# Performance work log

Measured on AMD Instinct MI355X. Metric: run time of the kernel, lower is better.

## Reference

```python
import jax, jax.numpy as jnp
import numpy as np

B, Q, P, H, NH, NKV, D = 8, 16, 4096, 4096, 32, 8, 128
ROPE_BASE = 10000.0


def setup_inputs() -> dict:
    key = jax.random.key(0)
    ks = jax.random.split(key, 8)
    hidden_states = jax.random.normal(ks[0], (B, Q, H), dtype=jnp.float32)
    past_key = jax.random.normal(ks[1], (B, NKV, P, D), dtype=jnp.float32)
    past_value = jax.random.normal(ks[2], (B, NKV, P, D), dtype=jnp.float32)
    # draft tokens continue right after the cached prefix
    position_ids = jnp.broadcast_to(P + jnp.arange(Q, dtype=jnp.int64), (B, Q))
    attention_bias = jnp.zeros((B, 1, Q, P + Q), dtype=jnp.float32)
    s = 0.02
    Wq = jax.random.normal(ks[3], (H, NH * D), dtype=jnp.float32) * s
    Wk = jax.random.normal(ks[4], (H, NKV * D), dtype=jnp.float32) * s
    Wv = jax.random.normal(ks[5], (H, NKV * D), dtype=jnp.float32) * s
    Wo = jax.random.normal(ks[6], (NH * D, H), dtype=jnp.float32) * s
    return {"hidden_states": hidden_states, "position_ids": position_ids,
            "past_key": past_key, "past_value": past_value,
            "attention_bias": attention_bias, "Wq": Wq, "Wk": Wk, "Wv": Wv, "Wo": Wo}


def _rope_cos_sin(position_ids, dtype):
    # inv_freq over even dims, GPT-NeoX layout: angles repeated (concat) over halves
    inv_freq = 1.0 / (ROPE_BASE ** (jnp.arange(0, D, 2, dtype=jnp.float32) / D))
    ang = position_ids.astype(jnp.float32)[:, :, None] * inv_freq  # [B,Q,D/2]
    emb = jnp.concatenate([ang, ang], axis=-1)  # [B,Q,D]
    cos = jnp.cos(emb).astype(dtype)[:, None, :, :]  # [B,1,Q,D]
    sin = jnp.sin(emb).astype(dtype)[:, None, :, :]
    return cos, sin


def _rotate_half(x):
    x1, x2 = jnp.split(x, 2, axis=-1)
    return jnp.concatenate([-x2, x1], axis=-1)


def reference(hidden_states, position_ids, past_key, past_value, attention_bias,
              Wq, Wk, Wv, Wo):
    b, q_len, _ = hidden_states.shape
    n_kv = past_key.shape[1]
    groups = NH // n_kv
    # projections
    q = (hidden_states @ Wq).reshape(b, q_len, NH, D).transpose(0, 2, 1, 3)   # [B,NH,Q,D]
    k = (hidden_states @ Wk).reshape(b, q_len, n_kv, D).transpose(0, 2, 1, 3)  # [B,NKV,Q,D]
    v = (hidden_states @ Wv).reshape(b, q_len, n_kv, D).transpose(0, 2, 1, 3)
    # RoPE
    cos, sin = _rope_cos_sin(position_ids, hidden_states.dtype)
    q = q * cos + _rotate_half(q) * sin
    k = k * cos + _rotate_half(k) * sin
    # KV-cache append
    k_all = jnp.concatenate([past_key, k], axis=2)    # [B,NKV,S,D]
    v_all = jnp.concatenate([past_value, v], axis=2)
    # GQA attention: group query heads per kv head instead of repeat_interleave
    qg = q.reshape(b, n_kv, groups, q_len, D)
    scale = 1.0 / jnp.sqrt(jnp.asarray(D, dtype=hidden_states.dtype))
    scores = jnp.einsum('bkgqd,bksd->bkgqs', qg, k_all) * scale
    scores = scores + attention_bias[:, :, None, :, :]  # bias [B,1,Q,S] -> broadcast
    probs = jax.nn.softmax(scores, axis=-1)
    out = jnp.einsum('bkgqs,bksd->bkgqd', probs, v_all)  # [B,NKV,G,Q,D]
    out = out.reshape(b, NH, q_len, D).transpose(0, 2, 1, 3).reshape(b, q_len, NH * D)
    return out @ Wo
```

## Files before the change

### kernel.cpp

```cpp
#include <hip/hip_runtime.h>
#include <hip/hip_bf16.h>

#define NB 8
#define NQ 16
#define NP 4096
#define NHID 4096
#define NHEADS 32
#define NKVH 8
#define NG 4
#define ND 128
#define NM 128
#define NSEQ 4112
#define N_QKV 6144
#define SPLITK 8
#define NS 8

typedef __attribute__((ext_vector_type(8))) short bf16x8;
typedef __attribute__((ext_vector_type(4))) float f32x4;

__device__ __forceinline__ unsigned short f2bf(float f) {
  unsigned int u = __float_as_uint(f);
  u = (u + 0x7FFFu + ((u >> 16) & 1u)) >> 16;
  return (unsigned short)u;
}

__device__ __forceinline__ unsigned cvtpk(float lo, float hi) {
  unsigned r;
  asm("v_cvt_pk_bf16_f32 %0, %1, %2" : "=v"(r) : "v"(lo), "v"(hi));
  return r;
}

__device__ __forceinline__ float bf2f(unsigned short u) {
  return __uint_as_float(((unsigned)u) << 16);
}

#define TRREAD(dst, a32) \
  asm volatile("ds_read_b64_tr_b16 %0, %1" : "=v"(dst) : "v"(a32))
#define LGKM0() asm volatile("s_waitcnt lgkmcnt(0)" ::: "memory")
#define SBAR()                              \
  do {                                      \
    __builtin_amdgcn_sched_barrier(0);      \
    __builtin_amdgcn_s_barrier();           \
    __builtin_amdgcn_sched_barrier(0);      \
  } while (0)

__global__ __launch_bounds__(256) void k_cvt(const float* __restrict__ x,
                                             unsigned short* __restrict__ y, int n4) {
  int i = blockIdx.x * 256 + threadIdx.x;
  if (i >= n4) return;
  f32x4 v = ((const f32x4*)x)[i];
  uint2 o;
  o.x = cvtpk(v[0], v[1]);
  o.y = cvtpk(v[2], v[3]);
  ((uint2*)y)[i] = o;
}

template<int CT>
__global__ __launch_bounds__(256) void k_gemm(
    const unsigned short* __restrict__ A, int lda,
    const float* __restrict__ W0, const float* __restrict__ W1,
    const float* __restrict__ W2, int nw0, int nw1, int N, int KS,
    float* __restrict__ part) {
  constexpr int BN = CT * 32;
  constexpr int NT = CT * 2;
  constexpr int NW4 = BN / 4;
  constexpr int KST = 256 / NW4;
  __shared__ __align__(16) char Bl[8 * NT * 128];
  int n0 = blockIdx.x * BN;
  int k0 = blockIdx.y * KS;
  const float* Wp; int ldw, ncol;
  if (n0 < nw0)      { Wp = W0; ldw = nw0;       ncol = n0; }
  else if (n0 < nw1) { Wp = W1; ldw = nw1 - nw0; ncol = n0 - nw0; }
  else               { Wp = W2; ldw = N - nw1;   ncol = n0 - nw1; }
  int tid = threadIdx.x, lane = tid & 63, wid = tid >> 6;
  int r16 = lane & 15, hi = lane >> 4;
  int wr = wid >> 1, wc = wid & 1;
  int n4 = tid & (NW4 - 1), krow = tid / NW4;
  unsigned lb = (unsigned)(uintptr_t)(void*)Bl;

  f32x4 acc[4][CT];
#pragma unroll
  for (int i = 0; i < 4; ++i)
#pragma unroll
    for (int j = 0; j < CT; ++j) acc[i][j] = {0.f, 0.f, 0.f, 0.f};

  f32x4 cur[CT], nxt[CT];
#pragma unroll
  for (int r = 0; r < CT; ++r) {
    cur[r] = *(const f32x4*)&Wp[(size_t)(k0 + krow + r * KST) * ldw + ncol + n4 * 4];
    nxt[r] = cur[r];
  }

  for (int kk = 0; kk < KS; kk += 32) {
    SBAR();
    if (kk + 32 < KS) {
#pragma unroll
      for (int r = 0; r < CT; ++r)
        nxt[r] = *(const f32x4*)&Wp[(size_t)(k0 + kk + 32 + krow + r * KST) * ldw + ncol + n4 * 4];
    }
#pragma unroll
    for (int r = 0; r < CT; ++r) {
      int k = krow + r * KST;
      uint2 u;
      u.x = cvtpk(cur[r][0], cur[r][1]);
      u.y = cvtpk(cur[r][2], cur[r][3]);
      *(uint2*)(Bl + ((k >> 2) * NT + (n4 >> 2)) * 128 + (k & 3) * 32 + (n4 & 3) * 8) = u;
    }
    LGKM0();
    SBAR();
    bf16x8 af[4];
#pragma unroll
    for (int rt = 0; rt < 4; ++rt)
      af[rt] = *(const bf16x8*)&A[(size_t)(wr * 64 + rt * 16 + r16) * lda + k0 + kk + hi * 8];
    unsigned long long rr[2 * CT];
#pragma unroll
    for (int ct = 0; ct < CT; ++ct) {
      int s1 = hi * (2 * NT) + wc * CT + ct;
      TRREAD(rr[ct * 2],     lb + s1 * 128 + r16 * 8);
      TRREAD(rr[ct * 2 + 1], lb + (s1 + NT) * 128 + r16 * 8);
    }
    LGKM0();
    __builtin_amdgcn_sched_barrier(0);
    __builtin_amdgcn_s_setprio(1);
#pragma unroll
    for (int ct = 0; ct < CT; ++ct) {
      union { unsigned long long u[2]; bf16x8 v; } cc;
      cc.u[0] = rr[ct * 2]; cc.u[1] = rr[ct * 2 + 1];
#pragma unroll
      for (int rt = 0; rt < 4; ++rt)
        acc[rt][ct] = __builtin_amdgcn_mfma_f32_16x16x32_bf16(af[rt], cc.v, acc[rt][ct], 0, 0, 0);
    }
    __builtin_amdgcn_s_setprio(0);
#pragma unroll
    for (int r = 0; r < CT; ++r) cur[r] = nxt[r];
  }
  float* po = part + (size_t)blockIdx.y * NM * N;
#pragma unroll
  for (int rt = 0; rt < 4; ++rt)
#pragma unroll
    for (int ct = 0; ct < CT; ++ct)
#pragma unroll
      for (int r = 0; r < 4; ++r) {
        int m = wr * 64 + rt * 16 + hi * 4 + r;
        int n = n0 + wc * CT * 16 + ct * 16 + r16;
        po[(size_t)m * N + n] = acc[rt][ct][r];
      }
}

__global__ __launch_bounds__(256) void k_rope(
    const float* __restrict__ part, const void* __restrict__ posv,
    unsigned short* __restrict__ qb, unsigned short* __restrict__ kb,
    unsigned short* __restrict__ vb) {
  int t = blockIdx.x * 256 + threadIdx.x;
  int d = t & 63;
  int rest = t >> 6;
  int h = rest % 48;
  int m = rest / 48;
  if (m >= NM) return;
  const int* p32 = (const int*)posv;
  const long long* p64 = (const long long*)posv;
  bool is64 = (p64[0] == (long long)p32[0]);
  int pos = is64 ? (int)p64[m] : p32[m];
  int b = m >> 4, q = m & 15;

  int c1, c2;
  if (h < 32)      { c1 = h * ND + d; }
  else if (h < 40) { c1 = NHID + (h - 32) * ND + d; }
  else             { c1 = NHID + 1024 + (h - 40) * ND + d; }
  c2 = c1 + 64;
  float x1 = 0.f, x2 = 0.f;
#pragma unroll
  for (int c = 0; c < SPLITK; ++c) {
    x1 += part[((size_t)c * NM + m) * N_QKV + c1];
    x2 += part[((size_t)c * NM + m) * N_QKV + c2];
  }
  if (h < 40) {
    float invf = __expf(-(float)d * 0.14391156831212787f);
    float th = (float)pos * invf;
    float cs = cosf(th), sn = sinf(th);
    float o1 = x1 * cs - x2 * sn;
    float o2 = x2 * cs + x1 * sn;
    if (h < 32) {
      o1 *= 0.08838834764831845f;
      o2 *= 0.08838834764831845f;
      int kv = h >> 2, g = h & 3;
      size_t base = ((((size_t)b * NKVH + kv) * NG + g) * NQ + q) * ND;
      qb[base + d] = f2bf(o1);
      qb[base + d + 64] = f2bf(o2);
    } else {
      int kvh = h - 32;
      size_t base = (((size_t)b * NKVH + kvh) * NQ + q) * ND;
      kb[base + d] = f2bf(o1);
      kb[base + d + 64] = f2bf(o2);
    }
  } else {
    int kvh = h - 40;
    size_t base = (((size_t)b * NKVH + kvh) * NQ + q) * ND;
    vb[base + d] = f2bf(x1);
    vb[base + d + 64] = f2bf(x2);
  }
}

template<int NSPL>
__global__ __launch_bounds__(256, 2) void k_attn(
    const unsigned short* __restrict__ qb, const unsigned short* __restrict__ kb,
    const unsigned short* __restrict__ vb, const float* __restrict__ pastK,
    const float* __restrict__ pastV, const float* __restrict__ bias,
    unsigned short* __restrict__ pout, float* __restrict__ pml) {
  __shared__ __align__(16) char lds[73728];
  char* Pl = lds + 65536;
  constexpr int KEYS = NP / NSPL;
  constexpr int NSUB = KEYS / 64;
  int bkv = blockIdx.x;
  int split = blockIdx.y;
  int b = bkv >> 3, kv = bkv & 7;
  int tid = threadIdx.x, lane = tid & 63, wid = tid >> 6;
  int r16 = lane & 15, hi = lane >> 4;

  const unsigned short* qbase = qb + ((((size_t)b * NKVH + kv) * NG + wid) * NQ) * ND;
  bf16x8 qf[4];
#pragma unroll
  for (int kd = 0; kd < 4; ++kd)
    qf[kd] = *(const bf16x8*)&qbase[r16 * ND + kd * 32 + hi * 8];

  float m_run[4], l_run[4];
  f32x4 oacc[8];
#pragma unroll
  for (int r = 0; r < 4; ++r) { m_run[r] = -1e30f; l_run[r] = 0.f; }
#pragma unroll
  for (int dt = 0; dt < 8; ++dt) oacc[dt] = {0.f, 0.f, 0.f, 0.f};

  int s0 = split * KEYS;
  const float* Kg = pastK + ((size_t)(b * NKVH + kv) * NP + s0) * ND;
  const float* Vg = pastV + ((size_t)(b * NKVH + kv) * NP + s0) * ND;
  const float* biasrow = bias + (size_t)(b * NQ) * NSEQ;
  int d4 = tid & 31, sr = tid >> 5;
  bool last = (split == NSPL - 1);

  f32x4 rwK[8], rwV[8];
  float bcur[16], bn[16], bt[4];
  bf16x8 tk, tv;

  f32x4 sc[4];
  auto qk_softmax = [&](char* Kl, const float* bv, bool tail) {
    __builtin_amdgcn_s_setprio(1);
#pragma unroll
    for (int ct = 0; ct < 4; ++ct) {
      f32x4 a = {0.f, 0.f, 0.f, 0.f};
      int s = ct * 16 + r16;
#pragma unroll
      for (int kd = 0; kd < 4; ++kd) {
        bf16x8 kf = *(const bf16x8*)(Kl + s * 256 + ((kd * 64 + hi * 16) ^ ((s & 7) << 4)));
        a = __builtin_amdgcn_mfma_f32_16x16x32_bf16(qf[kd], kf, a, 0, 0, 0);
      }
      sc[ct] = a;
    }
    __builtin_amdgcn_s_setprio(0);
#pragma unroll
    for (int ct = 0; ct < 4; ++ct)
#pragma unroll
      for (int r = 0; r < 4; ++r) {
        if (!tail)          sc[ct][r] += bv[ct * 4 + r];
        else if (ct == 0)   sc[ct][r] += bv[r];
        else                sc[ct][r] = -1e30f;
      }
    float mnew[4], fac[4], rs[4];
#pragma unroll
    for (int r = 0; r < 4; ++r) {
      float v = fmaxf(fmaxf(sc[0][r], sc[1][r]), fmaxf(sc[2][r], sc[3][r]));
      v = fmaxf(v, __shfl_xor(v, 1));
      v = fmaxf(v, __shfl_xor(v, 2));
      v = fmaxf(v, __shfl_xor(v, 4));
      v = fmaxf(v, __shfl_xor(v, 8));
      mnew[r] = fmaxf(m_run[r], v);
      fac[r] = __expf(m_run[r] - mnew[r]);
      m_run[r] = mnew[r];
      rs[r] = 0.f;
    }
#pragma unroll
    for (int ct = 0; ct < 4; ++ct)
#pragma unroll
      for (int r = 0; r < 4; ++r) {
        float p = __expf(sc[ct][r] - mnew[r]);
        rs[r] += p;
        int q = hi * 4 + r, j = ct * 16 + r16;
        *(unsigned short*)(Pl + wid * 2048 + q * 128 + ((j * 2) ^ ((q & 7) << 4))) = f2bf(p);
      }
#pragma unroll
    for (int r = 0; r < 4; ++r) {
      float s = rs[r];
      s += __shfl_xor(s, 1);
      s += __shfl_xor(s, 2);
      s += __shfl_xor(s, 4);
      s += __shfl_xor(s, 8);
      l_run[r] = l_run[r] * fac[r] + s;
    }
#pragma unroll
    for (int dt = 0; dt < 8; ++dt)
#pragma unroll
      for (int r = 0; r < 4; ++r) oacc[dt][r] *= fac[r];
  };

  auto pv = [&](char* Vl) {
    unsigned vb32 = (unsigned)(uintptr_t)(void*)Vl;
#pragma unroll
    for (int kt = 0; kt < 2; ++kt) {
      bf16x8 pa = *(const bf16x8*)(Pl + wid * 2048 + r16 * 128 +
                                   ((kt * 64 + hi * 16) ^ ((r16 & 7) << 4)));
#pragma unroll
      for (int dh = 0; dh < 2; ++dh) {
        unsigned long long rr[8];
#pragma unroll
        for (int dq = 0; dq < 4; ++dq) {
          int sA = hi * 16 + kt * 64 + dh * 4 + dq;
          TRREAD(rr[dq * 2],     vb32 + sA * 128 + r16 * 8);
          TRREAD(rr[dq * 2 + 1], vb32 + (sA + 8) * 128 + r16 * 8);
        }
        LGKM0();
        __builtin_amdgcn_sched_barrier(0);
        __builtin_amdgcn_s_setprio(1);
#pragma unroll
        for (int dq = 0; dq < 4; ++dq) {
          union { unsigned long long u[2]; bf16x8 v; } cc;
          cc.u[0] = rr[dq * 2]; cc.u[1] = rr[dq * 2 + 1];
          oacc[dh * 4 + dq] = __builtin_amdgcn_mfma_f32_16x16x32_bf16(pa, cc.v, oacc[dh * 4 + dq], 0, 0, 0);
        }
        __builtin_amdgcn_s_setprio(0);
      }
    }
  };

#pragma unroll
  for (int it = 0; it < 8; ++it)
    rwK[it] = *(const f32x4*)&Kg[(size_t)(sr + it * 8) * ND + d4 * 4];
#pragma unroll
  for (int it = 0; it < 8; ++it)
    rwV[it] = *(const f32x4*)&Vg[(size_t)(sr + it * 8) * ND + d4 * 4];
#pragma unroll
  for (int ct = 0; ct < 4; ++ct)
#pragma unroll
    for (int r = 0; r < 4; ++r)
      bcur[ct * 4 + r] = biasrow[(size_t)(hi * 4 + r) * NSEQ + s0 + ct * 16 + r16];
#pragma unroll
  for (int it = 0; it < 8; ++it) {
    int s = sr + it * 8;
    uint2 u;
    u.x = cvtpk(rwK[it][0], rwK[it][1]); u.y = cvtpk(rwK[it][2], rwK[it][3]);
    *(uint2*)(lds + s * 256 + ((d4 * 8) ^ ((s & 7) << 4))) = u;
  }
#pragma unroll
  for (int it = 0; it < 8; ++it) {
    int s = sr + it * 8;
    uint2 u;
    u.x = cvtpk(rwV[it][0], rwV[it][1]); u.y = cvtpk(rwV[it][2], rwV[it][3]);
    *(uint2*)(lds + 32768 + ((s >> 2) * 8 + (d4 >> 2)) * 128 + (s & 3) * 32 + (d4 & 3) * 8) = u;
  }
  LGKM0();

  int cur = 0;
  for (int sub = 0; sub < NSUB; ++sub) {
    bool pf = (sub + 1 < NSUB);
    if (pf) {
      const float* Kn = Kg + (size_t)(sub + 1) * 64 * ND;
      const float* Vn = Vg + (size_t)(sub + 1) * 64 * ND;
#pragma unroll
      for (int it = 0; it < 8; ++it)
        rwK[it] = *(const f32x4*)&Kn[(size_t)(sr + it * 8) * ND + d4 * 4];
#pragma unroll
      for (int it = 0; it < 8; ++it)
        rwV[it] = *(const f32x4*)&Vn[(size_t)(sr + it * 8) * ND + d4 * 4];
#pragma unroll
      for (int ct = 0; ct < 4; ++ct)
#pragma unroll
        for (int r = 0; r < 4; ++r)
          bn[ct * 4 + r] = biasrow[(size_t)(hi * 4 + r) * NSEQ + s0 + (sub + 1) * 64 + ct * 16 + r16];
    } else if (last) {
      int s = tid >> 4, d8 = tid & 15;
      const unsigned short* Kn = kb + (((size_t)b * NKVH + kv) * NQ) * ND;
      const unsigned short* Vn = vb + (((size_t)b * NKVH + kv) * NQ) * ND;
      tk = *(const bf16x8*)&Kn[s * ND + d8 * 8];
      tv = *(const bf16x8*)&Vn[s * ND + d8 * 8];
#pragma unroll
      for (int r = 0; r < 4; ++r)
        bt[r] = biasrow[(size_t)(hi * 4 + r) * NSEQ + NP + r16];
    }
    SBAR();
    qk_softmax(lds + cur * 16384, bcur, false);
    pv(lds + 32768 + cur * 16384);
    if (pf) {
#pragma unroll
      for (int it = 0; it < 8; ++it) {
        int s = sr + it * 8;
        uint2 u;
        u.x = cvtpk(rwK[it][0], rwK[it][1]); u.y = cvtpk(rwK[it][2], rwK[it][3]);
        *(uint2*)(lds + (cur ^ 1) * 16384 + s * 256 + ((d4 * 8) ^ ((s & 7) << 4))) = u;
      }
#pragma unroll
      for (int it = 0; it < 8; ++it) {
        int s = sr + it * 8;
        uint2 u;
        u.x = cvtpk(rwV[it][0], rwV[it][1]); u.y = cvtpk(rwV[it][2], rwV[it][3]);
        *(uint2*)(lds + 32768 + (cur ^ 1) * 16384 +
                  ((s >> 2) * 8 + (d4 >> 2)) * 128 + (s & 3) * 32 + (d4 & 3) * 8) = u;
      }
#pragma unroll
      for (int i = 0; i < 16; ++i) bcur[i] = bn[i];
      LGKM0();
      cur ^= 1;
    } else if (last) {
      int s = tid >> 4, d8 = tid & 15;
      *(bf16x8*)(lds + (cur ^ 1) * 16384 + s * 256 + ((d8 * 16) ^ ((s & 7) << 4))) = tk;
      *(bf16x8*)(lds + 32768 + (cur ^ 1) * 16384 +
                 ((s >> 2) * 8 + (d8 >> 1)) * 128 + (s & 3) * 32 + (d8 & 1) * 16) = tv;
      LGKM0();
      cur ^= 1;
    }
  }
  if (last) {
    SBAR();
    qk_softmax(lds + cur * 16384, bt, true);
    pv(lds + 32768 + cur * 16384);
  }

  SBAR();
  char* My = lds + wid * 4096;
#pragma unroll
  for (int dt = 0; dt < 8; ++dt)
#pragma unroll
    for (int r = 0; r < 4; ++r)
      *(unsigned short*)(My + (hi * 4 + r) * 256 + (dt * 16 + r16) * 2) = f2bf(oacc[dt][r]);
  LGKM0();
  size_t rowbase = ((size_t)(b * NKVH + kv) * NG + wid) * NQ;
  unsigned short* po = pout + ((size_t)split * (NB * NKVH * NG * NQ) + rowbase) * ND;
#pragma unroll
  for (int it = 0; it < 4; ++it) {
    int row = it * 4 + (lane >> 4);
    uint4 vv = *(uint4*)(My + row * 256 + r16 * 16);
    *(uint4*)&po[(size_t)row * ND + r16 * 8] = vv;
  }
  if (r16 == 0) {
#pragma unroll
    for (int r = 0; r < 4; ++r) {
      size_t idx = ((size_t)split * (NB * NKVH * NG * NQ) + rowbase + hi * 4 + r) * 2;
      pml[idx] = m_run[r];
      pml[idx + 1] = l_run[r];
    }
  }
}

template<int NSPL>
__global__ __launch_bounds__(256) void k_combine(
    const unsigned short* __restrict__ pout, const float* __restrict__ pml,
    unsigned short* __restrict__ Aatt) {
  const int NROW = NB * NKVH * NG * NQ;
  int row = blockIdx.x * 2 + (threadIdx.x >> 7);
  int d = threadIdx.x & 127;
  float mv[NSPL], lv[NSPL];
  float M = -1e30f;
#pragma unroll
  for (int c = 0; c < NSPL; ++c) {
    mv[c] = pml[((size_t)c * NROW + row) * 2];
    lv[c] = pml[((size_t)c * NROW + row) * 2 + 1];
    M = fmaxf(M, mv[c]);
  }
  float L = 0.f, acc = 0.f;
#pragma unroll
  for (int c = 0; c < NSPL; ++c) {
    float w = __expf(mv[c] - M);
    L += lv[c] * w;
    acc += bf2f(pout[((size_t)c * NROW + row) * ND + d]) * w;
  }
  float o = acc / L;
  int q = row & 15, g = (row >> 4) & 3, kvh = (row >> 6) & 7, b = row >> 9;
  Aatt[(size_t)(b * NQ + q) * NHID + (kvh * NG + g) * ND + d] = f2bf(o);
}

__global__ __launch_bounds__(256) void k_red(const float* __restrict__ part,
                                             float* __restrict__ out) {
  int i = blockIdx.x * 256 + threadIdx.x;
  float s = 0.f;
#pragma unroll
  for (int c = 0; c < SPLITK; ++c) s += part[(size_t)c * (NM * NHID) + i];
  out[i] = s;
}

extern "C" void kernel_launch(void* const* d_in, const int* in_sizes, int n_in,
                              void* d_out, int out_size, void* d_ws, size_t ws_size,
                              hipStream_t stream) {
  const float* hidden = (const float*)d_in[0];
  const void* pos = d_in[1];
  const float* pastK = (const float*)d_in[2];
  const float* pastV = (const float*)d_in[3];
  const float* bias = (const float*)d_in[4];
  const float* Wq = (const float*)d_in[5];
  const float* Wk = (const float*)d_in[6];
  const float* Wv = (const float*)d_in[7];
  const float* Wo = (const float*)d_in[8];
  float* out = (float*)d_out;

  char* ws = (char*)d_ws;
  size_t off = 0;
  auto alloc = [&](size_t bytes) {
    char* p = ws + off;
    off += (bytes + 255) & ~(size_t)255;
    return p;
  };
  unsigned short* hb   = (unsigned short*)alloc((size_t)NM * NHID * 2);
  unsigned short* qb   = (unsigned short*)alloc((size_t)NB * NKVH * NG * NQ * ND * 2);
  unsigned short* kb   = (unsigned short*)alloc((size_t)NB * NKVH * NQ * ND * 2);
  unsigned short* vb   = (unsigned short*)alloc((size_t)NB * NKVH * NQ * ND * 2);
  unsigned short* Aatt = (unsigned short*)alloc((size_t)NM * NHID * 2);

  size_t mlB = (size_t)NS * 8192 * 2 * 4;
  float* pml = (float*)(ws + off);
  unsigned short* pout = (unsigned short*)(ws + off + mlB);
  float* part = (float*)(ws + off);

  k_cvt<<<512, 256, 0, stream>>>(hidden, hb, NM * NHID / 4);
  k_gemm<2><<<dim3(96, SPLITK), 256, 0, stream>>>(hb, NHID, Wq, Wk, Wv, 4096, 5120,
                                                  N_QKV, NHID / SPLITK, part);
  k_rope<<<1536, 256, 0, stream>>>(part, pos, qb, kb, vb);
  k_attn<NS><<<dim3(64, NS), 256, 0, stream>>>(qb, kb, vb, pastK, pastV, bias, pout, pml);
  k_combine<NS><<<4096, 256, 0, stream>>>(pout, pml, Aatt);
  k_gemm<2><<<dim3(64, SPLITK), 256, 0, stream>>>(Aatt, NHID, Wo, Wo, Wo, 4096, 8192,
                                                  NHID, NHID / SPLITK, part);
  k_red<<<2048, 256, 0, stream>>>(part, out);
}
```

Measured before the change: 158.1 us.

## Deepen K prefetch to two tiles and interleave V conversion with compute

Restructures the attention split loop's software pipeline. K tiles and bias are now prefetched two tiles ahead into alternating register sets, while V for the next tile is issued just before QK and converted to LDS after PV. K conversion for the next tile is placed between QK-softmax and PV, so global-load latency overlaps more compute. The cost is higher register pressure from the extra K and bias register sets plus a fully unrolled loop, which may lower occupancy or cause spills.

```diff
diff --git a/kernel.cpp b/kernel.cpp
--- a/kernel.cpp
+++ b/kernel.cpp
@@ -237,9 +237,47 @@
   int d4 = tid & 31, sr = tid >> 5;
   bool last = (split == NSPL - 1);
 
-  f32x4 rwK[8], rwV[8];
-  float bcur[16], bn[16], bt[4];
+  f32x4 kRA[8], kRB[8], vR[8];
+  float bRA[16], bRB[16], bt[4];
   bf16x8 tk, tv;
+
+  auto kissue = [&](f32x4 (&kr)[8], int tile) {
+    const float* Kn = Kg + (size_t)tile * 64 * ND;
+#pragma unroll
+    for (int it = 0; it < 8; ++it)
+      kr[it] = *(const f32x4*)&Kn[(size_t)(sr + it * 8) * ND + d4 * 4];
+  };
+  auto vissue = [&](int tile) {
+    const float* Vn = Vg + (size_t)tile * 64 * ND;
+#pragma unroll
+    for (int it = 0; it < 8; ++it)
+      vR[it] = *(const f32x4*)&Vn[(size_t)(sr + it * 8) * ND + d4 * 4];
+  };
+  auto bissue = [&](float (&br)[16], int tile) {
+#pragma unroll
+    for (int ct = 0; ct < 4; ++ct)
+#pragma unroll
+      for (int r = 0; r < 4; ++r)
+        br[ct * 4 + r] = biasrow[(size_t)(hi * 4 + r) * NSEQ + s0 + tile * 64 + ct * 16 + r16];
+  };
+  auto kconv = [&](f32x4 (&kr)[8], char* Kl) {
+#pragma unroll
+    for (int it = 0; it < 8; ++it) {
+      int s = sr + it * 8;
+      uint2 u;
+      u.x = cvtpk(kr[it][0], kr[it][1]); u.y = cvtpk(kr[it][2], kr[it][3]);
+      *(uint2*)(Kl + s * 256 + ((d4 * 8) ^ ((s & 7) << 4))) = u;
+    }
+  };
+  auto vconv = [&](char* Vl) {
+#pragma unroll
+    for (int it = 0; it < 8; ++it) {
+      int s = sr + it * 8;
+      uint2 u;
+      u.x = cvtpk(vR[it][0], vR[it][1]); u.y = cvtpk(vR[it][2], vR[it][3]);
+      *(uint2*)(Vl + ((s >> 2) * 8 + (d4 >> 2)) * 128 + (s & 3) * 32 + (d4 & 3) * 8) = u;
+    }
+  };
 
   f32x4 sc[4];
   auto qk_softmax = [&](char* Kl, const float* bv, bool tail) {
@@ -330,51 +368,35 @@
     }
   };
 
-#pragma unroll
-  for (int it = 0; it < 8; ++it)
-    rwK[it] = *(const f32x4*)&Kg[(size_t)(sr + it * 8) * ND + d4 * 4];
-#pragma unroll
-  for (int it = 0; it < 8; ++it)
-    rwV[it] = *(const f32x4*)&Vg[(size_t)(sr + it * 8) * ND + d4 * 4];
-#pragma unroll
-  for (int ct = 0; ct < 4; ++ct)
-#pragma unroll
-    for (int r = 0; r < 4; ++r)
-      bcur[ct * 4 + r] = biasrow[(size_t)(hi * 4 + r) * NSEQ + s0 + ct * 16 + r16];
-#pragma unroll
-  for (int it = 0; it < 8; ++it) {
-    int s = sr + it * 8;
-    uint2 u;
-    u.x = cvtpk(rwK[it][0], rwK[it][1]); u.y = cvtpk(rwK[it][2], rwK[it][3]);
-    *(uint2*)(lds + s * 256 + ((d4 * 8) ^ ((s & 7) << 4))) = u;
-  }
-#pragma unroll
-  for (int it = 0; it < 8; ++it) {
-    int s = sr + it * 8;
-    uint2 u;
-    u.x = cvtpk(rwV[it][0], rwV[it][1]); u.y = cvtpk(rwV[it][2], rwV[it][3]);
-    *(uint2*)(lds + 32768 + ((s >> 2) * 8 + (d4 >> 2)) * 128 + (s & 3) * 32 + (d4 & 3) * 8) = u;
-  }
+  kissue(kRA, 0);
+  vissue(0);
+  kconv(kRA, lds + 0);
+  vconv(lds + 32768);
+  kissue(kRB, 1);
+  bissue(bRA, 0);
+  bissue(bRB, 1);
   LGKM0();
 
-  int cur = 0;
+#pragma unroll
   for (int sub = 0; sub < NSUB; ++sub) {
-    bool pf = (sub + 1 < NSUB);
-    if (pf) {
-      const float* Kn = Kg + (size_t)(sub + 1) * 64 * ND;
-      const float* Vn = Vg + (size_t)(sub + 1) * 64 * ND;
-#pragma unroll
-      for (int it = 0; it < 8; ++it)
-        rwK[it] = *(const f32x4*)&Kn[(size_t)(sr + it * 8) * ND + d4 * 4];
-#pragma unroll
-      for (int it = 0; it < 8; ++it)
-        rwV[it] = *(const f32x4*)&Vn[(size_t)(sr + it * 8) * ND + d4 * 4];
-#pragma unroll
-      for (int ct = 0; ct < 4; ++ct)
-#pragma unroll
-        for (int r = 0; r < 4; ++r)
-          bn[ct * 4 + r] = biasrow[(size_t)(hi * 4 + r) * NSEQ + s0 + (sub + 1) * 64 + ct * 16 + r16];
+    const int p = sub & 1;
+    char* KlC = lds + p * 16384;
+    char* VlC = lds + 32768 + p * 16384;
+    char* KlN = lds + (p ^ 1) * 16384;
+    char* VlN = lds + 32768 + (p ^ 1) * 16384;
+    SBAR();
+    if (sub + 1 < NSUB) vissue(sub + 1);
+    qk_softmax(KlC, p ? bRB : bRA, false);
+    if (sub + 1 < NSUB) {
+      if (p) kconv(kRA, KlN); else kconv(kRB, KlN);
     } else if (last) {
+      int s = tid >> 4, d8 = tid & 15;
+      *(bf16x8*)(KlN + s * 256 + ((d8 * 16) ^ ((s & 7) << 4))) = tk;
+    }
+    if (sub + 2 < NSUB) {
+      if (p) { kissue(kRB, sub + 2); bissue(bRB, sub + 2); }
+      else   { kissue(kRA, sub + 2); bissue(bRA, sub + 2); }
+    } else if (sub + 2 == NSUB && last) {
       int s = tid >> 4, d8 = tid & 15;
       const unsigned short* Kn = kb + (((size_t)b * NKVH + kv) * NQ) * ND;
       const unsigned short* Vn = vb + (((size_t)b * NKVH + kv) * NQ) * ND;
@@ -384,42 +406,19 @@
       for (int r = 0; r < 4; ++r)
         bt[r] = biasrow[(size_t)(hi * 4 + r) * NSEQ + NP + r16];
     }
-    SBAR();
-    qk_softmax(lds + cur * 16384, bcur, false);
-    pv(lds + 32768 + cur * 16384);
-    if (pf) {
-#pragma unroll
-      for (int it = 0; it < 8; ++it) {
-        int s = sr + it * 8;
-        uint2 u;
-        u.x = cvtpk(rwK[it][0], rwK[it][1]); u.y = cvtpk(rwK[it][2], rwK[it][3]);
-        *(uint2*)(lds + (cur ^ 1) * 16384 + s * 256 + ((d4 * 8) ^ ((s & 7) << 4))) = u;
-      }
-#pragma unroll
-      for (int it = 0; it < 8; ++it) {
-        int s = sr + it * 8;
-        uint2 u;
-        u.x = cvtpk(rwV[it][0], rwV[it][1]); u.y = cvtpk(rwV[it][2], rwV[it][3]);
-        *(uint2*)(lds + 32768 + (cur ^ 1) * 16384 +
-                  ((s >> 2) * 8 + (d4 >> 2)) * 128 + (s & 3) * 32 + (d4 & 3) * 8) = u;
-      }
-#pragma unroll
-      for (int i = 0; i < 16; ++i) bcur[i] = bn[i];
-      LGKM0();
-      cur ^= 1;
+    pv(VlC);
+    if (sub + 1 < NSUB) {
+      vconv(VlN);
     } else if (last) {
       int s = tid >> 4, d8 = tid & 15;
-      *(bf16x8*)(lds + (cur ^ 1) * 16384 + s * 256 + ((d8 * 16) ^ ((s & 7) << 4))) = tk;
-      *(bf16x8*)(lds + 32768 + (cur ^ 1) * 16384 +
-                 ((s >> 2) * 8 + (d8 >> 1)) * 128 + (s & 3) * 32 + (d8 & 1) * 16) = tv;
-      LGKM0();
-      cur ^= 1;
-    }
+      *(bf16x8*)(VlN + ((s >> 2) * 8 + (d8 >> 1)) * 128 + (s & 3) * 32 + (d8 & 1) * 16) = tv;
+    }
+    LGKM0();
   }
   if (last) {
     SBAR();
-    qk_softmax(lds + cur * 16384, bt, true);
-    pv(lds + 32768 + cur * 16384);
+    qk_softmax(lds + (NSUB & 1) * 16384, bt, true);
+    pv(lds + 32768 + (NSUB & 1) * 16384);
   }
 
   SBAR();
```

After: 241.6 us. +52.8%, slower.
